# Kernel tuning notes

Measured on AMD Instinct MI355X. Metric: run time of the kernel, lower is better.

## Reference

```python
import jax, jax.numpy as jnp
import numpy as np

N = 8192
PERCEPTION = 0.2
SEP_DIST = 0.02
ACC_SCALE = 1.0
ACC_MAX = 1.0
EPS = 1e-08


def setup_inputs() -> dict:
    key = jax.random.key(0)
    k1, k2, k3 = jax.random.split(key, 3)
    position = jax.random.uniform(k1, (N, 2), dtype=jnp.float32)  # boids live in [0,1]^2 torus
    velocity = jax.random.normal(k2, (N, 2), dtype=jnp.float32) * 0.05
    noise = jax.random.uniform(k3, (N, 2), dtype=jnp.float32, minval=-1.0, maxval=1.0)
    return {
        "position": position,
        "velocity": velocity,
        "noise": noise,
        "separation_weight": jnp.float32(4.5),
        "alignment_weight": jnp.float32(0.65),
        "cohesion_weight": jnp.float32(0.75),
        "noise_scale": jnp.float32(0.05),
    }


def _normalize(v):
    # per-row normalize, matching module's _normalize
    norm = jnp.maximum(jnp.linalg.norm(v, axis=-1, keepdims=True), EPS)
    return v / norm


def reference(position, velocity, noise, separation_weight, alignment_weight, cohesion_weight, noise_scale):
    # Toroidal vector from boid i to boid j: diff[i, j, :]  (shape [N, N, 2])
    diff = position[None, :, :] - position[:, None, :]
    diff = jnp.where(diff > 0.5, diff - 1.0, diff)
    diff = jnp.where(diff < -0.5, diff + 1.0, diff)
    dist2 = jnp.sum(diff * diff, axis=-1)  # [N, N]

    not_self = ~jnp.eye(N, dtype=bool)

    # Separation: sum of -toroidal_vector over too-close neighbors, normalized
    sep_mask = not_self & (dist2 <= SEP_DIST ** 2)
    steer_sep = -jnp.sum(jnp.where(sep_mask[..., None], diff, 0.0), axis=1)
    steer_sep = _normalize(steer_sep)

    # Perception mask shared by alignment and cohesion
    perc_mask = not_self & (dist2 <= PERCEPTION ** 2)
    cnt = jnp.sum(perc_mask, axis=1, dtype=position.dtype)[:, None]  # [N, 1]

    # Alignment: mean neighbor velocity minus own velocity, normalized
    vel_avg = jnp.einsum("ij,jd->id", perc_mask.astype(position.dtype), velocity) / cnt
    steer_align = _normalize(vel_avg - velocity)

    # Cohesion: mean toroidal vector to neighbors, normalized
    pos_avg = jnp.sum(jnp.where(perc_mask[..., None], diff, 0.0), axis=1) / cnt
    steer_coh = _normalize(pos_avg)

    acc = (separation_weight * steer_sep
           + alignment_weight * steer_align
           + cohesion_weight * steer_coh)
    acc = acc * ACC_SCALE
    acc = acc + noise_scale * noise

    # clip by norm per boid
    norm = jnp.linalg.norm(acc, axis=-1, keepdims=True)
    acc = jnp.where(norm > ACC_MAX, acc * ACC_MAX / jnp.maximum(norm, EPS), acc)
    return acc
```

## Files before the change

kernel.cpp:

```cpp
#include <hip/hip_runtime.h>
#include <math.h>

#define N_BOIDS 8192
typedef float f32x2 __attribute__((ext_vector_type(2)));
typedef float f32x4 __attribute__((ext_vector_type(4)));

constexpr int   BLOCK       = 1024;
constexpr int   JSPLIT      = 2;
constexpr int   GROUPS      = (BLOCK / 64) / JSPLIT;
constexpr int   I_PER_GROUP = 2;
constexpr int   I_PER_BLOCK = GROUPS * I_PER_GROUP;
constexpr int   TILE        = 4096;
constexpr int   NTILES      = N_BOIDS / TILE;
constexpr int   K_PER_WAVE  = TILE / 64 / JSPLIT;
constexpr float SEP_R2  = 4.0000000000000008e-04f;
constexpr float PERC_R2 = 4.0000000000000001e-02f;
constexpr float EPSF    = 1e-08f;

__device__ __forceinline__ void finalize_boid(
    int i, const f32x2* __restrict__ vel, const f32x2* __restrict__ noise,
    float ws, float wa, float wc, float wn,
    float sx, float sy, float vx, float vy, float cx, float cy, float cntall,
    float* __restrict__ out)
{
    const float cnt = cntall - 1.0f;

    float ns  = fmaxf(sqrtf(sx * sx + sy * sy), EPSF);
    float ssx = sx / ns, ssy = sy / ns;

    const f32x2 vi = vel[i];
    float vax = (vx - vi.x) / cnt - vi.x;
    float vay = (vy - vi.y) / cnt - vi.y;
    float na  = fmaxf(sqrtf(vax * vax + vay * vay), EPSF);
    float sax = vax / na, say = vay / na;

    float pax = cx / cnt, pay = cy / cnt;
    float nc  = fmaxf(sqrtf(pax * pax + pay * pay), EPSF);
    float scx = pax / nc, scy = pay / nc;

    float ax = ws * ssx + wa * sax + wc * scx;
    float ay = ws * ssy + wa * say + wc * scy;
    const f32x2 nz = noise[i];
    ax += wn * nz.x;
    ay += wn * nz.y;

    const float nn = sqrtf(ax * ax + ay * ay);
    if (nn > 1.0f) {
        const float s = 1.0f / fmaxf(nn, EPSF);
        ax *= s;
        ay *= s;
    }
    out[2 * i]     = ax;
    out[2 * i + 1] = ay;
}

__global__ __launch_bounds__(BLOCK, 8) void boids_kernel(
    const f32x2* __restrict__ pos,
    const f32x2* __restrict__ vel,
    const f32x2* __restrict__ noise,
    const float* __restrict__ w_sep,
    const float* __restrict__ w_ali,
    const float* __restrict__ w_coh,
    const float* __restrict__ w_noise,
    float* __restrict__ out)
{
    __shared__ f32x4 tile[TILE];
    __shared__ float comb[GROUPS][16];

    const int tid  = threadIdx.x;
    const int lane = tid & 63;
    const int wid  = tid >> 6;
    const int g    = wid >> 1;
    const int h    = wid & 1;
    const int i0   = blockIdx.x * I_PER_BLOCK + g * I_PER_GROUP;

    const f32x2 P0 = pos[i0];
    const f32x2 P1 = pos[i0 + 1];
    const float vperc = PERC_R2;
    const float vsep  = SEP_R2;

    float n0  = 0.f, s0x = 0.f, s0y = 0.f, v0x = 0.f, v0y = 0.f, c0x = 0.f, c0y = 0.f;
    float n1  = 0.f, s1x = 0.f, s1y = 0.f, v1x = 0.f, v1y = 0.f, c1x = 0.f, c1y = 0.f;

    for (int t = 0; t < NTILES; ++t) {
        const f32x4* gp = reinterpret_cast<const f32x4*>(pos) + t * (TILE / 2);
        const f32x4* gv = reinterpret_cast<const f32x4*>(vel) + t * (TILE / 2);
#pragma unroll
        for (int c = 0; c < TILE / 2 / BLOCK; ++c) {
            const int idx  = tid + c * BLOCK;
            const f32x4 pp = gp[idx];
            const f32x4 vv = gv[idx];
            f32x4 t0; t0.x = pp.x; t0.y = pp.y; t0.z = vv.x; t0.w = vv.y;
            f32x4 t1; t1.x = pp.z; t1.y = pp.w; t1.z = vv.z; t1.w = vv.w;
            tile[2 * idx]     = t0;
            tile[2 * idx + 1] = t1;
        }
        __syncthreads();

        const int kbase = h * K_PER_WAVE;
#pragma unroll 8
        for (int k = 0; k < K_PER_WAVE; ++k) {
            const f32x4 q = tile[lane + (kbase + k) * 64];
            float dx0, dy0, dx1, dy1, ta, tb, tc, m;
            unsigned long long ka, kb, kc;
            asm(
                "v_sub_f32   %[dx0], %[qx], %[p0x]\n\t"
                "v_sub_f32   %[dy0], %[qy], %[p0y]\n\t"
                "v_sub_f32   %[dx1], %[qx], %[p1x]\n\t"
                "v_sub_f32   %[dy1], %[qy], %[p1y]\n\t"
                "v_rndne_f32 %[ta], %[dx0]\n\t"
                "v_rndne_f32 %[tb], %[dy0]\n\t"
                "v_sub_f32   %[dx0], %[dx0], %[ta]\n\t"
                "v_sub_f32   %[dy0], %[dy0], %[tb]\n\t"
                "v_rndne_f32 %[ta], %[dx1]\n\t"
                "v_rndne_f32 %[tb], %[dy1]\n\t"
                "v_sub_f32   %[dx1], %[dx1], %[ta]\n\t"
                "v_sub_f32   %[dy1], %[dy1], %[tb]\n\t"
                "v_mul_f32   %[ta], %[dx0], %[dx0]\n\t"
                "v_mul_f32   %[tb], %[dy0], %[dy0]\n\t"
                "v_add_f32   %[ta], %[ta], %[tb]\n\t"
                "v_mul_f32   %[tb], %[dx1], %[dx1]\n\t"
                "v_mul_f32   %[tc], %[dy1], %[dy1]\n\t"
                "v_add_f32   %[tb], %[tb], %[tc]\n\t"
                "v_cmp_ge_f32 vcc, %[vperc], %[ta]\n\t"
                "v_cndmask_b32 %[m], 0, 1.0, vcc\n\t"
                "v_add_f32   %[n0], %[n0], %[m]\n\t"
                "v_fmac_f32  %[v0x], %[m], %[qz]\n\t"
                "v_fmac_f32  %[v0y], %[m], %[qw]\n\t"
                "v_fmac_f32  %[c0x], %[m], %[dx0]\n\t"
                "v_fmac_f32  %[c0y], %[m], %[dy0]\n\t"
                "v_cmp_ge_f32 vcc, %[vperc], %[tb]\n\t"
                "v_cndmask_b32 %[m], 0, 1.0, vcc\n\t"
                "v_add_f32   %[n1], %[n1], %[m]\n\t"
                "v_fmac_f32  %[v1x], %[m], %[qz]\n\t"
                "v_fmac_f32  %[v1y], %[m], %[qw]\n\t"
                "v_fmac_f32  %[c1x], %[m], %[dx1]\n\t"
                "v_fmac_f32  %[c1y], %[m], %[dy1]\n\t"
                "v_cmp_ge_f32 %[ka], %[vsep], %[ta]\n\t"
                "v_cmp_ge_f32 %[kb], %[vsep], %[tb]\n\t"
                "s_or_b64    %[kc], %[ka], %[kb]\n\t"
                "s_cbranch_scc0 Lsep%=\n\t"
                "v_cndmask_b32 %[m], 0, 1.0, %[ka]\n\t"
                "v_fma_f32   %[s0x], -%[m], %[dx0], %[s0x]\n\t"
                "v_fma_f32   %[s0y], -%[m], %[dy0], %[s0y]\n\t"
                "v_cndmask_b32 %[m], 0, 1.0, %[kb]\n\t"
                "v_fma_f32   %[s1x], -%[m], %[dx1], %[s1x]\n\t"
                "v_fma_f32   %[s1y], -%[m], %[dy1], %[s1y]\n\t"
                "Lsep%=:"
                : [dx0] "=&v"(dx0), [dy0] "=&v"(dy0),
                  [dx1] "=&v"(dx1), [dy1] "=&v"(dy1),
                  [ta] "=&v"(ta), [tb] "=&v"(tb), [tc] "=&v"(tc), [m] "=&v"(m),
                  [ka] "=&s"(ka), [kb] "=&s"(kb), [kc] "=&s"(kc),
                  [n0] "+v"(n0), [s0x] "+v"(s0x), [s0y] "+v"(s0y),
                  [v0x] "+v"(v0x), [v0y] "+v"(v0y),
                  [c0x] "+v"(c0x), [c0y] "+v"(c0y),
                  [n1] "+v"(n1), [s1x] "+v"(s1x), [s1y] "+v"(s1y),
                  [v1x] "+v"(v1x), [v1y] "+v"(v1y),
                  [c1x] "+v"(c1x), [c1y] "+v"(c1y)
                : [qx] "v"(q.x), [qy] "v"(q.y), [qz] "v"(q.z), [qw] "v"(q.w),
                  [p0x] "v"(P0.x), [p0y] "v"(P0.y),
                  [p1x] "v"(P1.x), [p1y] "v"(P1.y),
                  [vperc] "v"(vperc), [vsep] "v"(vsep)
                : "vcc", "scc");
        }
        __syncthreads();
    }

#pragma unroll
    for (int mlev = 1; mlev < 64; mlev <<= 1) {
        n0  += __shfl_xor(n0,  mlev);
        s0x += __shfl_xor(s0x, mlev);  s0y += __shfl_xor(s0y, mlev);
        v0x += __shfl_xor(v0x, mlev);  v0y += __shfl_xor(v0y, mlev);
        c0x += __shfl_xor(c0x, mlev);  c0y += __shfl_xor(c0y, mlev);
        n1  += __shfl_xor(n1,  mlev);
        s1x += __shfl_xor(s1x, mlev);  s1y += __shfl_xor(s1y, mlev);
        v1x += __shfl_xor(v1x, mlev);  v1y += __shfl_xor(v1y, mlev);
        c1x += __shfl_xor(c1x, mlev);  c1y += __shfl_xor(c1y, mlev);
    }

    if (h == 1 && lane == 0) {
        comb[g][0]  = s0x; comb[g][1]  = s0y;
        comb[g][2]  = v0x; comb[g][3]  = v0y;
        comb[g][4]  = c0x; comb[g][5]  = c0y;
        comb[g][6]  = n0;
        comb[g][7]  = s1x; comb[g][8]  = s1y;
        comb[g][9]  = v1x; comb[g][10] = v1y;
        comb[g][11] = c1x; comb[g][12] = c1y;
        comb[g][13] = n1;
    }
    __syncthreads();

    if (h == 0 && lane < I_PER_GROUP) {
        float sx = s0x, sy = s0y, vx = v0x, vy = v0y, cx = c0x, cy = c0y, cc = n0;
        if (lane == 1) {
            sx = s1x; sy = s1y; vx = v1x; vy = v1y; cx = c1x; cy = c1y; cc = n1;
        }
        const float* cb = &comb[g][lane * 7];
        sx += cb[0]; sy += cb[1]; vx += cb[2]; vy += cb[3];
        cx += cb[4]; cy += cb[5]; cc += cb[6];
        const float ws = w_sep[0], wa = w_ali[0], wc = w_coh[0], wn = w_noise[0];
        finalize_boid(i0 + lane, vel, noise, ws, wa, wc, wn,
                      sx, sy, vx, vy, cx, cy, cc, out);
    }
}

extern "C" void kernel_launch(void* const* d_in, const int* in_sizes, int n_in,
                              void* d_out, int out_size, void* d_ws, size_t ws_size,
                              hipStream_t stream) {
    const f32x2* pos     = (const f32x2*)d_in[0];
    const f32x2* vel     = (const f32x2*)d_in[1];
    const f32x2* noise   = (const f32x2*)d_in[2];
    const float* w_sep   = (const float*)d_in[3];
    const float* w_ali   = (const float*)d_in[4];
    const float* w_coh   = (const float*)d_in[5];
    const float* w_noise = (const float*)d_in[6];
    float* out = (float*)d_out;

    const int grid = N_BOIDS / I_PER_BLOCK;
    boids_kernel<<<grid, BLOCK, 0, stream>>>(pos, vel, noise, w_sep, w_ali,
                                             w_coh, w_noise, out);
}
```

Baseline: 35.47 us.

## Replace all-pairs scan with uniform-grid cell binning and neighbor-cell traversal

Adds three preprocessing kernels that build a 16x16 uniform grid: a per-block histogram, a scan, and a scatter that writes boids in cell order with packed pos/vel and their original indices. The main kernel then visits only the cells within the perception radius of each boid pair, loading neighbors straight from global memory and masking out partial chunks. This is meant to cut the O(N^2) pair work to roughly the fraction of the torus covered by the perception window (about 5x5 of 16x16 cells). In exchange it costs three extra launches, a serial scan, an O(CHUNK) rank loop in the scatter, and uncoalesced neighbor reads. An all-pairs fallback runs when the workspace is too small.

```diff
diff --git a/kernel.cpp b/kernel.cpp
--- a/kernel.cpp
+++ b/kernel.cpp
@@ -5,58 +5,123 @@
 typedef float f32x2 __attribute__((ext_vector_type(2)));
 typedef float f32x4 __attribute__((ext_vector_type(4)));
 
-constexpr int   BLOCK       = 1024;
-constexpr int   JSPLIT      = 2;
-constexpr int   GROUPS      = (BLOCK / 64) / JSPLIT;
-constexpr int   I_PER_GROUP = 2;
-constexpr int   I_PER_BLOCK = GROUPS * I_PER_GROUP;
-constexpr int   TILE        = 4096;
-constexpr int   NTILES      = N_BOIDS / TILE;
-constexpr int   K_PER_WAVE  = TILE / 64 / JSPLIT;
+constexpr int   NC     = 16;
+constexpr int   NCELL  = NC * NC;
+constexpr float MARG   = 0.2002f;
+constexpr int   CHUNK  = 256;
+constexpr int   NBLK   = N_BOIDS / CHUNK;
+constexpr size_t HIST_OFF = 0;
+constexpr size_t BASE_OFF = 32768;
+constexpr size_t CS_OFF   = 65536;
+constexpr size_t SORT_OFF = 69632;
+constexpr size_t SIDX_OFF = 200704;
+constexpr size_t WS_NEED  = 233472;
+
 constexpr float SEP_R2  = 4.0000000000000008e-04f;
 constexpr float PERC_R2 = 4.0000000000000001e-02f;
 constexpr float EPSF    = 1e-08f;
 
-__device__ __forceinline__ void finalize_boid(
-    int i, const f32x2* __restrict__ vel, const f32x2* __restrict__ noise,
+__device__ __forceinline__ int cell_of(float px, float py) {
+    int cx = (int)(px * 16.0f); cx = cx > 15 ? 15 : (cx < 0 ? 0 : cx);
+    int cy = (int)(py * 16.0f); cy = cy > 15 ? 15 : (cy < 0 ? 0 : cy);
+    return cy * NC + cx;
+}
+
+__global__ __launch_bounds__(CHUNK) void cell_hist(
+    const float* __restrict__ pos, int* __restrict__ hist)
+{
+    __shared__ int h[NCELL];
+    const int tid = threadIdx.x;
+    h[tid] = 0;
+    __syncthreads();
+    const int i = blockIdx.x * CHUNK + tid;
+    atomicAdd(&h[cell_of(pos[2 * i], pos[2 * i + 1])], 1);
+    __syncthreads();
+    hist[blockIdx.x * NCELL + tid] = h[tid];
+}
+
+__global__ __launch_bounds__(NCELL) void cell_scan(
+    const int* __restrict__ hist, int* __restrict__ base, int* __restrict__ cs)
+{
+    __shared__ int tot[NCELL];
+    __shared__ int sc[NCELL + 1];
+    const int c = threadIdx.x;
+    int hh[NBLK];
+    int t = 0;
+#pragma unroll
+    for (int b = 0; b < NBLK; ++b) { hh[b] = hist[b * NCELL + c]; t += hh[b]; }
+    tot[c] = t;
+    __syncthreads();
+    if (c == 0) {
+        int run = 0;
+        for (int k = 0; k < NCELL; ++k) { sc[k] = run; run += tot[k]; }
+        sc[NCELL] = run;
+    }
+    __syncthreads();
+    cs[c] = sc[c];
+    if (c == 0) cs[NCELL] = sc[NCELL];
+    int run2 = sc[c];
+#pragma unroll
+    for (int b = 0; b < NBLK; ++b) { base[b * NCELL + c] = run2; run2 += hh[b]; }
+}
+
+__global__ __launch_bounds__(CHUNK) void cell_scatter(
+    const float* __restrict__ pos, const float* __restrict__ vel,
+    const int* __restrict__ base, float4* __restrict__ sorted4,
+    int* __restrict__ sidx)
+{
+    __shared__ int cid[CHUNK];
+    __shared__ int lbase[NCELL];
+    const int tid = threadIdx.x;
+    const int b   = blockIdx.x;
+    const int i   = b * CHUNK + tid;
+    const float px = pos[2 * i], py = pos[2 * i + 1];
+    const int c = cell_of(px, py);
+    cid[tid]   = c;
+    lbase[tid] = base[b * NCELL + tid];
+    __syncthreads();
+    int rank = 0;
+    for (int t2 = 0; t2 < tid; ++t2) rank += (cid[t2] == c) ? 1 : 0;
+    const int slot = lbase[c] + rank;
+    float4 o; o.x = px; o.y = py; o.z = vel[2 * i]; o.w = vel[2 * i + 1];
+    sorted4[slot] = o;
+    sidx[slot]    = i;
+}
+
+__device__ __forceinline__ void finalize_core(
+    float vix, float viy, const f32x2 nz,
     float ws, float wa, float wc, float wn,
     float sx, float sy, float vx, float vy, float cx, float cy, float cntall,
-    float* __restrict__ out)
+    float* __restrict__ out, int orig)
 {
     const float cnt = cntall - 1.0f;
-
     float ns  = fmaxf(sqrtf(sx * sx + sy * sy), EPSF);
     float ssx = sx / ns, ssy = sy / ns;
-
-    const f32x2 vi = vel[i];
-    float vax = (vx - vi.x) / cnt - vi.x;
-    float vay = (vy - vi.y) / cnt - vi.y;
+    float vax = (vx - vix) / cnt - vix;
+    float vay = (vy - viy) / cnt - viy;
     float na  = fmaxf(sqrtf(vax * vax + vay * vay), EPSF);
     float sax = vax / na, say = vay / na;
-
     float pax = cx / cnt, pay = cy / cnt;
     float nc  = fmaxf(sqrtf(pax * pax + pay * pay), EPSF);
     float scx = pax / nc, scy = pay / nc;
-
     float ax = ws * ssx + wa * sax + wc * scx;
     float ay = ws * ssy + wa * say + wc * scy;
-    const f32x2 nz = noise[i];
     ax += wn * nz.x;
     ay += wn * nz.y;
-
     const float nn = sqrtf(ax * ax + ay * ay);
     if (nn > 1.0f) {
         const float s = 1.0f / fmaxf(nn, EPSF);
         ax *= s;
         ay *= s;
     }
-    out[2 * i]     = ax;
-    out[2 * i + 1] = ay;
-}
-
-__global__ __launch_bounds__(BLOCK, 8) void boids_kernel(
-    const f32x2* __restrict__ pos,
-    const f32x2* __restrict__ vel,
+    out[2 * orig]     = ax;
+    out[2 * orig + 1] = ay;
+}
+
+__global__ __launch_bounds__(256, 4) void boids_main(
+    const float4* __restrict__ sorted4,
+    const int* __restrict__ sidx,
+    const int* __restrict__ cs,
     const f32x2* __restrict__ noise,
     const float* __restrict__ w_sep,
     const float* __restrict__ w_ali,
@@ -64,106 +129,111 @@
     const float* __restrict__ w_noise,
     float* __restrict__ out)
 {
-    __shared__ f32x4 tile[TILE];
-    __shared__ float comb[GROUPS][16];
-
-    const int tid  = threadIdx.x;
+    __shared__ int cs_l[NCELL + 1];
+    const int tid = threadIdx.x;
+    cs_l[tid] = cs[tid];
+    if (tid == 0) cs_l[NCELL] = cs[NCELL];
+    __syncthreads();
+
     const int lane = tid & 63;
     const int wid  = tid >> 6;
-    const int g    = wid >> 1;
-    const int h    = wid & 1;
-    const int i0   = blockIdx.x * I_PER_BLOCK + g * I_PER_GROUP;
-
-    const f32x2 P0 = pos[i0];
-    const f32x2 P1 = pos[i0 + 1];
+    const int i0   = (blockIdx.x * 4 + wid) * 2;
+
+    const float4 I0 = sorted4[i0];
+    const float4 I1 = sorted4[i0 + 1];
     const float vperc = PERC_R2;
     const float vsep  = SEP_R2;
 
-    float n0  = 0.f, s0x = 0.f, s0y = 0.f, v0x = 0.f, v0y = 0.f, c0x = 0.f, c0y = 0.f;
-    float n1  = 0.f, s1x = 0.f, s1y = 0.f, v1x = 0.f, v1y = 0.f, c1x = 0.f, c1y = 0.f;
-
-    for (int t = 0; t < NTILES; ++t) {
-        const f32x4* gp = reinterpret_cast<const f32x4*>(pos) + t * (TILE / 2);
-        const f32x4* gv = reinterpret_cast<const f32x4*>(vel) + t * (TILE / 2);
-#pragma unroll
-        for (int c = 0; c < TILE / 2 / BLOCK; ++c) {
-            const int idx  = tid + c * BLOCK;
-            const f32x4 pp = gp[idx];
-            const f32x4 vv = gv[idx];
-            f32x4 t0; t0.x = pp.x; t0.y = pp.y; t0.z = vv.x; t0.w = vv.y;
-            f32x4 t1; t1.x = pp.z; t1.y = pp.w; t1.z = vv.z; t1.w = vv.w;
-            tile[2 * idx]     = t0;
-            tile[2 * idx + 1] = t1;
+    const float xmn = fminf(I0.x, I1.x), xmx = fmaxf(I0.x, I1.x);
+    const float ymn = fminf(I0.y, I1.y), ymx = fmaxf(I0.y, I1.y);
+    const int cx0 = (int)floorf((xmn - MARG) * 16.0f);
+    const int cx1 = (int)floorf((xmx + MARG) * 16.0f);
+    const int cy0 = (int)floorf((ymn - MARG) * 16.0f);
+    const int cy1 = (int)floorf((ymx + MARG) * 16.0f);
+    int nx = cx1 - cx0 + 1; if (nx > NC) nx = NC;
+    int ny = cy1 - cy0 + 1; if (ny > NC) ny = NC;
+
+    float n0 = 0.f, s0x = 0.f, s0y = 0.f, v0x = 0.f, v0y = 0.f, c0x = 0.f, c0y = 0.f;
+    float n1 = 0.f, s1x = 0.f, s1y = 0.f, v1x = 0.f, v1y = 0.f, c1x = 0.f, c1y = 0.f;
+
+    for (int r = 0; r < ny; ++r) {
+        const int ry      = (cy0 + r) & (NC - 1);
+        const int rowbase = ry * NC;
+        const int a0      = cx0 & (NC - 1);
+        const int lenA    = (nx < NC - a0) ? nx : (NC - a0);
+        const int lenB    = nx - lenA;
+        const int sA = cs_l[rowbase + a0];
+        const int eA = cs_l[rowbase + a0 + lenA];
+        const int sB = cs_l[rowbase];
+        const int eB = cs_l[rowbase + lenB];
+        for (int seg = 0; seg < 2; ++seg) {
+            const int js = seg ? sB : sA;
+            const int je = seg ? eB : eA;
+            for (int j0 = js; j0 < je; j0 += 64) {
+                const int   rem = je - j0;
+                const int   jj  = (lane < rem) ? (j0 + lane) : j0;
+                const float inv = (lane < rem) ? 0.0f : 1e9f;
+                const float4 q  = sorted4[jj];
+                float dx0, dy0, dx1, dy1, ta, tb, tc, m;
+                asm(
+                    "v_sub_f32   %[dx0], %[qx], %[p0x]\n\t"
+                    "v_sub_f32   %[dy0], %[qy], %[p0y]\n\t"
+                    "v_sub_f32   %[dx1], %[qx], %[p1x]\n\t"
+                    "v_sub_f32   %[dy1], %[qy], %[p1y]\n\t"
+                    "v_rndne_f32 %[ta], %[dx0]\n\t"
+                    "v_rndne_f32 %[tb], %[dy0]\n\t"
+                    "v_sub_f32   %[dx0], %[dx0], %[ta]\n\t"
+                    "v_sub_f32   %[dy0], %[dy0], %[tb]\n\t"
+                    "v_rndne_f32 %[ta], %[dx1]\n\t"
+                    "v_rndne_f32 %[tb], %[dy1]\n\t"
+                    "v_sub_f32   %[dx1], %[dx1], %[ta]\n\t"
+                    "v_sub_f32   %[dy1], %[dy1], %[tb]\n\t"
+                    "v_mul_f32   %[ta], %[dx0], %[dx0]\n\t"
+                    "v_mul_f32   %[tb], %[dy0], %[dy0]\n\t"
+                    "v_add_f32   %[ta], %[ta], %[tb]\n\t"
+                    "v_max_f32   %[ta], %[ta], %[inv]\n\t"
+                    "v_mul_f32   %[tb], %[dx1], %[dx1]\n\t"
+                    "v_mul_f32   %[tc], %[dy1], %[dy1]\n\t"
+                    "v_add_f32   %[tb], %[tb], %[tc]\n\t"
+                    "v_max_f32   %[tb], %[tb], %[inv]\n\t"
+                    "v_cmp_ge_f32 vcc, %[vperc], %[ta]\n\t"
+                    "v_cndmask_b32 %[m], 0, 1.0, vcc\n\t"
+                    "v_add_f32   %[n0], %[n0], %[m]\n\t"
+                    "v_fmac_f32  %[v0x], %[m], %[qz]\n\t"
+                    "v_fmac_f32  %[v0y], %[m], %[qw]\n\t"
+                    "v_fmac_f32  %[c0x], %[m], %[dx0]\n\t"
+                    "v_fmac_f32  %[c0y], %[m], %[dy0]\n\t"
+                    "v_cmp_ge_f32 vcc, %[vperc], %[tb]\n\t"
+                    "v_cndmask_b32 %[m], 0, 1.0, vcc\n\t"
+                    "v_add_f32   %[n1], %[n1], %[m]\n\t"
+                    "v_fmac_f32  %[v1x], %[m], %[qz]\n\t"
+                    "v_fmac_f32  %[v1y], %[m], %[qw]\n\t"
+                    "v_fmac_f32  %[c1x], %[m], %[dx1]\n\t"
+                    "v_fmac_f32  %[c1y], %[m], %[dy1]\n\t"
+                    "v_cmp_ge_f32 vcc, %[vsep], %[ta]\n\t"
+                    "v_cndmask_b32 %[m], 0, 1.0, vcc\n\t"
+                    "v_fma_f32   %[s0x], -%[m], %[dx0], %[s0x]\n\t"
+                    "v_fma_f32   %[s0y], -%[m], %[dy0], %[s0y]\n\t"
+                    "v_cmp_ge_f32 vcc, %[vsep], %[tb]\n\t"
+                    "v_cndmask_b32 %[m], 0, 1.0, vcc\n\t"
+                    "v_fma_f32   %[s1x], -%[m], %[dx1], %[s1x]\n\t"
+                    "v_fma_f32   %[s1y], -%[m], %[dy1], %[s1y]\n\t"
+                    : [dx0] "=&v"(dx0), [dy0] "=&v"(dy0),
+                      [dx1] "=&v"(dx1), [dy1] "=&v"(dy1),
+                      [ta] "=&v"(ta), [tb] "=&v"(tb), [tc] "=&v"(tc), [m] "=&v"(m),
+                      [n0] "+v"(n0), [s0x] "+v"(s0x), [s0y] "+v"(s0y),
+                      [v0x] "+v"(v0x), [v0y] "+v"(v0y),
+                      [c0x] "+v"(c0x), [c0y] "+v"(c0y),
+                      [n1] "+v"(n1), [s1x] "+v"(s1x), [s1y] "+v"(s1y),
+                      [v1x] "+v"(v1x), [v1y] "+v"(v1y),
+                      [c1x] "+v"(c1x), [c1y] "+v"(c1y)
+                    : [qx] "v"(q.x), [qy] "v"(q.y), [qz] "v"(q.z), [qw] "v"(q.w),
+                      [p0x] "v"(I0.x), [p0y] "v"(I0.y),
+                      [p1x] "v"(I1.x), [p1y] "v"(I1.y),
+                      [vperc] "v"(vperc), [vsep] "v"(vsep), [inv] "v"(inv)
+                    : "vcc");
+            }
         }
-        __syncthreads();
-
-        const int kbase = h * K_PER_WAVE;
-#pragma unroll 8
-        for (int k = 0; k < K_PER_WAVE; ++k) {
-            const f32x4 q = tile[lane + (kbase + k) * 64];
-            float dx0, dy0, dx1, dy1, ta, tb, tc, m;
-            unsigned long long ka, kb, kc;
-            asm(
-                "v_sub_f32   %[dx0], %[qx], %[p0x]\n\t"
-                "v_sub_f32   %[dy0], %[qy], %[p0y]\n\t"
-                "v_sub_f32   %[dx1], %[qx], %[p1x]\n\t"
-                "v_sub_f32   %[dy1], %[qy], %[p1y]\n\t"
-                "v_rndne_f32 %[ta], %[dx0]\n\t"
-                "v_rndne_f32 %[tb], %[dy0]\n\t"
-                "v_sub_f32   %[dx0], %[dx0], %[ta]\n\t"
-                "v_sub_f32   %[dy0], %[dy0], %[tb]\n\t"
-                "v_rndne_f32 %[ta], %[dx1]\n\t"
-                "v_rndne_f32 %[tb], %[dy1]\n\t"
-                "v_sub_f32   %[dx1], %[dx1], %[ta]\n\t"
-                "v_sub_f32   %[dy1], %[dy1], %[tb]\n\t"
-                "v_mul_f32   %[ta], %[dx0], %[dx0]\n\t"
-                "v_mul_f32   %[tb], %[dy0], %[dy0]\n\t"
-                "v_add_f32   %[ta], %[ta], %[tb]\n\t"
-                "v_mul_f32   %[tb], %[dx1], %[dx1]\n\t"
-                "v_mul_f32   %[tc], %[dy1], %[dy1]\n\t"
-                "v_add_f32   %[tb], %[tb], %[tc]\n\t"
-                "v_cmp_ge_f32 vcc, %[vperc], %[ta]\n\t"
-                "v_cndmask_b32 %[m], 0, 1.0, vcc\n\t"
-                "v_add_f32   %[n0], %[n0], %[m]\n\t"
-                "v_fmac_f32  %[v0x], %[m], %[qz]\n\t"
-                "v_fmac_f32  %[v0y], %[m], %[qw]\n\t"
-                "v_fmac_f32  %[c0x], %[m], %[dx0]\n\t"
-                "v_fmac_f32  %[c0y], %[m], %[dy0]\n\t"
-                "v_cmp_ge_f32 vcc, %[vperc], %[tb]\n\t"
-                "v_cndmask_b32 %[m], 0, 1.0, vcc\n\t"
-                "v_add_f32   %[n1], %[n1], %[m]\n\t"
-                "v_fmac_f32  %[v1x], %[m], %[qz]\n\t"
-                "v_fmac_f32  %[v1y], %[m], %[qw]\n\t"
-                "v_fmac_f32  %[c1x], %[m], %[dx1]\n\t"
-                "v_fmac_f32  %[c1y], %[m], %[dy1]\n\t"
-                "v_cmp_ge_f32 %[ka], %[vsep], %[ta]\n\t"
-                "v_cmp_ge_f32 %[kb], %[vsep], %[tb]\n\t"
-                "s_or_b64    %[kc], %[ka], %[kb]\n\t"
-                "s_cbranch_scc0 Lsep%=\n\t"
-                "v_cndmask_b32 %[m], 0, 1.0, %[ka]\n\t"
-                "v_fma_f32   %[s0x], -%[m], %[dx0], %[s0x]\n\t"
-                "v_fma_f32   %[s0y], -%[m], %[dy0], %[s0y]\n\t"
-                "v_cndmask_b32 %[m], 0, 1.0, %[kb]\n\t"
-                "v_fma_f32   %[s1x], -%[m], %[dx1], %[s1x]\n\t"
-                "v_fma_f32   %[s1y], -%[m], %[dy1], %[s1y]\n\t"
-                "Lsep%=:"
-                : [dx0] "=&v"(dx0), [dy0] "=&v"(dy0),
-                  [dx1] "=&v"(dx1), [dy1] "=&v"(dy1),
-                  [ta] "=&v"(ta), [tb] "=&v"(tb), [tc] "=&v"(tc), [m] "=&v"(m),
-                  [ka] "=&s"(ka), [kb] "=&s"(kb), [kc] "=&s"(kc),
-                  [n0] "+v"(n0), [s0x] "+v"(s0x), [s0y] "+v"(s0y),
-                  [v0x] "+v"(v0x), [v0y] "+v"(v0y),
-                  [c0x] "+v"(c0x), [c0y] "+v"(c0y),
-                  [n1] "+v"(n1), [s1x] "+v"(s1x), [s1y] "+v"(s1y),
-                  [v1x] "+v"(v1x), [v1y] "+v"(v1y),
-                  [c1x] "+v"(c1x), [c1y] "+v"(c1y)
-                : [qx] "v"(q.x), [qy] "v"(q.y), [qz] "v"(q.z), [qw] "v"(q.w),
-                  [p0x] "v"(P0.x), [p0y] "v"(P0.y),
-                  [p1x] "v"(P1.x), [p1y] "v"(P1.y),
-                  [vperc] "v"(vperc), [vsep] "v"(vsep)
-                : "vcc", "scc");
-        }
-        __syncthreads();
     }
 
 #pragma unroll
@@ -178,37 +248,140 @@
         c1x += __shfl_xor(c1x, mlev);  c1y += __shfl_xor(c1y, mlev);
     }
 
-    if (h == 1 && lane == 0) {
-        comb[g][0]  = s0x; comb[g][1]  = s0y;
-        comb[g][2]  = v0x; comb[g][3]  = v0y;
-        comb[g][4]  = c0x; comb[g][5]  = c0y;
-        comb[g][6]  = n0;
-        comb[g][7]  = s1x; comb[g][8]  = s1y;
-        comb[g][9]  = v1x; comb[g][10] = v1y;
-        comb[g][11] = c1x; comb[g][12] = c1y;
-        comb[g][13] = n1;
-    }
-    __syncthreads();
-
-    if (h == 0 && lane < I_PER_GROUP) {
+    if (lane < 2) {
         float sx = s0x, sy = s0y, vx = v0x, vy = v0y, cx = c0x, cy = c0y, cc = n0;
+        float vix = I0.z, viy = I0.w;
         if (lane == 1) {
             sx = s1x; sy = s1y; vx = v1x; vy = v1y; cx = c1x; cy = c1y; cc = n1;
+            vix = I1.z; viy = I1.w;
         }
-        const float* cb = &comb[g][lane * 7];
-        sx += cb[0]; sy += cb[1]; vx += cb[2]; vy += cb[3];
-        cx += cb[4]; cy += cb[5]; cc += cb[6];
-        const float ws = w_sep[0], wa = w_ali[0], wc = w_coh[0], wn = w_noise[0];
-        finalize_boid(i0 + lane, vel, noise, ws, wa, wc, wn,
-                      sx, sy, vx, vy, cx, cy, cc, out);
+        const int orig = sidx[i0 + lane];
+        finalize_core(vix, viy, noise[orig],
+                      w_sep[0], w_ali[0], w_coh[0], w_noise[0],
+                      sx, sy, vx, vy, cx, cy, cc, out, orig);
+    }
+}
+
+constexpr int FB_BLOCK = 256;
+constexpr int FB_TILE  = 2048;
+
+__global__ __launch_bounds__(FB_BLOCK, 4) void boids_allpairs(
+    const f32x2* __restrict__ pos, const f32x2* __restrict__ vel,
+    const f32x2* __restrict__ noise,
+    const float* __restrict__ w_sep, const float* __restrict__ w_ali,
+    const float* __restrict__ w_coh, const float* __restrict__ w_noise,
+    float* __restrict__ out)
+{
+    __shared__ f32x4 tile[FB_TILE];
+    const int tid  = threadIdx.x;
+    const int lane = tid & 63;
+    const int wid  = tid >> 6;
+    const int i0   = (blockIdx.x * 4 + wid) * 2;
+    const f32x2 P0 = pos[i0];
+    const f32x2 P1 = pos[i0 + 1];
+    const float vperc = PERC_R2, vsep = SEP_R2;
+    float n0 = 0.f, s0x = 0.f, s0y = 0.f, v0x = 0.f, v0y = 0.f, c0x = 0.f, c0y = 0.f;
+    float n1 = 0.f, s1x = 0.f, s1y = 0.f, v1x = 0.f, v1y = 0.f, c1x = 0.f, c1y = 0.f;
+    for (int t = 0; t < N_BOIDS / FB_TILE; ++t) {
+        const f32x4* gp = reinterpret_cast<const f32x4*>(pos) + t * (FB_TILE / 2);
+        const f32x4* gv = reinterpret_cast<const f32x4*>(vel) + t * (FB_TILE / 2);
+#pragma unroll
+        for (int c = 0; c < FB_TILE / 2 / FB_BLOCK; ++c) {
+            const int idx  = tid + c * FB_BLOCK;
+            const f32x4 pp = gp[idx];
+            const f32x4 vv = gv[idx];
+            f32x4 t0; t0.x = pp.x; t0.y = pp.y; t0.z = vv.x; t0.w = vv.y;
+            f32x4 t1; t1.x = pp.z; t1.y = pp.w; t1.z = vv.z; t1.w = vv.w;
+            tile[2 * idx] = t0; tile[2 * idx + 1] = t1;
+        }
+        __syncthreads();
+#pragma unroll 8
+        for (int k = 0; k < FB_TILE / 64; ++k) {
+            const f32x4 q = tile[lane + k * 64];
+            float dx, dy, ta, tb, m;
+            asm("v_sub_f32 %[dx], %[qx], %[p0x]\n\t"
+                "v_sub_f32 %[dy], %[qy], %[p0y]\n\t"
+                "v_rndne_f32 %[ta], %[dx]\n\t"
+                "v_rndne_f32 %[tb], %[dy]\n\t"
+                "v_sub_f32 %[dx], %[dx], %[ta]\n\t"
+                "v_sub_f32 %[dy], %[dy], %[tb]\n\t"
+                "v_mul_f32 %[ta], %[dx], %[dx]\n\t"
+                "v_mul_f32 %[tb], %[dy], %[dy]\n\t"
+                "v_add_f32 %[ta], %[ta], %[tb]\n\t"
+                "v_cmp_ge_f32 vcc, %[vperc], %[ta]\n\t"
+                "v_cndmask_b32 %[m], 0, 1.0, vcc\n\t"
+                "v_add_f32 %[n0], %[n0], %[m]\n\t"
+                "v_fmac_f32 %[v0x], %[m], %[qz]\n\t"
+                "v_fmac_f32 %[v0y], %[m], %[qw]\n\t"
+                "v_fmac_f32 %[c0x], %[m], %[dx]\n\t"
+                "v_fmac_f32 %[c0y], %[m], %[dy]\n\t"
+                "v_cmp_ge_f32 vcc, %[vsep], %[ta]\n\t"
+                "v_cndmask_b32 %[m], 0, 1.0, vcc\n\t"
+                "v_fma_f32 %[s0x], -%[m], %[dx], %[s0x]\n\t"
+                "v_fma_f32 %[s0y], -%[m], %[dy], %[s0y]\n\t"
+                "v_sub_f32 %[dx], %[qx], %[p1x]\n\t"
+                "v_sub_f32 %[dy], %[qy], %[p1y]\n\t"
+                "v_rndne_f32 %[ta], %[dx]\n\t"
+                "v_rndne_f32 %[tb], %[dy]\n\t"
+                "v_sub_f32 %[dx], %[dx], %[ta]\n\t"
+                "v_sub_f32 %[dy], %[dy], %[tb]\n\t"
+                "v_mul_f32 %[ta], %[dx], %[dx]\n\t"
+                "v_mul_f32 %[tb], %[dy], %[dy]\n\t"
+                "v_add_f32 %[ta], %[ta], %[tb]\n\t"
+                "v_cmp_ge_f32 vcc, %[vperc], %[ta]\n\t"
+                "v_cndmask_b32 %[m], 0, 1.0, vcc\n\t"
+                "v_add_f32 %[n1], %[n1], %[m]\n\t"
+                "v_fmac_f32 %[v1x], %[m], %[qz]\n\t"
+                "v_fmac_f32 %[v1y], %[m], %[qw]\n\t"
+                "v_fmac_f32 %[c1x], %[m], %[dx]\n\t"
+                "v_fmac_f32 %[c1y], %[m], %[dy]\n\t"
+                "v_cmp_ge_f32 vcc, %[vsep], %[ta]\n\t"
+                "v_cndmask_b32 %[m], 0, 1.0, vcc\n\t"
+                "v_fma_f32 %[s1x], -%[m], %[dx], %[s1x]\n\t"
+                "v_fma_f32 %[s1y], -%[m], %[dy], %[s1y]\n\t"
+                : [dx] "=&v"(dx), [dy] "=&v"(dy), [ta] "=&v"(ta),
+                  [tb] "=&v"(tb), [m] "=&v"(m),
+                  [n0] "+v"(n0), [s0x] "+v"(s0x), [s0y] "+v"(s0y),
+                  [v0x] "+v"(v0x), [v0y] "+v"(v0y), [c0x] "+v"(c0x), [c0y] "+v"(c0y),
+                  [n1] "+v"(n1), [s1x] "+v"(s1x), [s1y] "+v"(s1y),
+                  [v1x] "+v"(v1x), [v1y] "+v"(v1y), [c1x] "+v"(c1x), [c1y] "+v"(c1y)
+                : [qx] "v"(q.x), [qy] "v"(q.y), [qz] "v"(q.z), [qw] "v"(q.w),
+                  [p0x] "v"(P0.x), [p0y] "v"(P0.y),
+                  [p1x] "v"(P1.x), [p1y] "v"(P1.y),
+                  [vperc] "v"(vperc), [vsep] "v"(vsep)
+                : "vcc");
+        }
+        __syncthreads();
+    }
+#pragma unroll
+    for (int mlev = 1; mlev < 64; mlev <<= 1) {
+        n0  += __shfl_xor(n0,  mlev);
+        s0x += __shfl_xor(s0x, mlev);  s0y += __shfl_xor(s0y, mlev);
+        v0x += __shfl_xor(v0x, mlev);  v0y += __shfl_xor(v0y, mlev);
+        c0x += __shfl_xor(c0x, mlev);  c0y += __shfl_xor(c0y, mlev);
+        n1  += __shfl_xor(n1,  mlev);
+        s1x += __shfl_xor(s1x, mlev);  s1y += __shfl_xor(s1y, mlev);
+        v1x += __shfl_xor(v1x, mlev);  v1y += __shfl_xor(v1y, mlev);
+        c1x += __shfl_xor(c1x, mlev);  c1y += __shfl_xor(c1y, mlev);
+    }
+    if (lane < 2) {
+        float sx = s0x, sy = s0y, vx = v0x, vy = v0y, cx = c0x, cy = c0y, cc = n0;
+        int i = i0;
+        if (lane == 1) {
+            sx = s1x; sy = s1y; vx = v1x; vy = v1y; cx = c1x; cy = c1y; cc = n1;
+            i = i0 + 1;
+        }
+        finalize_core(vel[i].x, vel[i].y, noise[i],
+                      w_sep[0], w_ali[0], w_coh[0], w_noise[0],
+                      sx, sy, vx, vy, cx, cy, cc, out, i);
     }
 }
 
 extern "C" void kernel_launch(void* const* d_in, const int* in_sizes, int n_in,
                               void* d_out, int out_size, void* d_ws, size_t ws_size,
                               hipStream_t stream) {
-    const f32x2* pos     = (const f32x2*)d_in[0];
-    const f32x2* vel     = (const f32x2*)d_in[1];
+    const float* pos_f   = (const float*)d_in[0];
+    const float* vel_f   = (const float*)d_in[1];
     const f32x2* noise   = (const f32x2*)d_in[2];
     const float* w_sep   = (const float*)d_in[3];
     const float* w_ali   = (const float*)d_in[4];
@@ -216,7 +389,21 @@
     const float* w_noise = (const float*)d_in[6];
     float* out = (float*)d_out;
 
-    const int grid = N_BOIDS / I_PER_BLOCK;
-    boids_kernel<<<grid, BLOCK, 0, stream>>>(pos, vel, noise, w_sep, w_ali,
-                                             w_coh, w_noise, out);
-}
+    if (ws_size >= WS_NEED) {
+        char* wsb = (char*)d_ws;
+        int*    hist    = (int*)(wsb + HIST_OFF);
+        int*    base    = (int*)(wsb + BASE_OFF);
+        int*    cs      = (int*)(wsb + CS_OFF);
+        float4* sorted4 = (float4*)(wsb + SORT_OFF);
+        int*    sidx    = (int*)(wsb + SIDX_OFF);
+        cell_hist<<<NBLK, CHUNK, 0, stream>>>(pos_f, hist);
+        cell_scan<<<1, NCELL, 0, stream>>>(hist, base, cs);
+        cell_scatter<<<NBLK, CHUNK, 0, stream>>>(pos_f, vel_f, base, sorted4, sidx);
+        boids_main<<<N_BOIDS / 8, 256, 0, stream>>>(
+            sorted4, sidx, cs, noise, w_sep, w_ali, w_coh, w_noise, out);
+    } else {
+        boids_allpairs<<<N_BOIDS / 8, FB_BLOCK, 0, stream>>>(
+            (const f32x2*)pos_f, (const f32x2*)vel_f, noise,
+            w_sep, w_ali, w_coh, w_noise, out);
+    }
+}
```

Result: slower. 41.13 us (+16.0%).
